# Performance work log

Measured on AMD Instinct MI355X. Metric: run time of the kernel, lower is better.

## Reference

```python
import jax, jax.numpy as jnp
import numpy as np

N, D = 8192, 256

def _gram_rbf(x, y, sigma):
    x2 = jnp.sum(x * x, axis=-1)                      # [N]
    y2 = jnp.sum(y * y, axis=-1)                      # [M]
    xy = jnp.einsum('nd,md->nm', x, y)                # [N,M] GEMM
    sq = x2[:, None] + y2[None, :] - 2.0 * xy
    return jnp.exp(-sq / sigma)

def setup_inputs() -> dict:
    key = jax.random.key(0)
    k1, k2 = jax.random.split(key)
    return {
        'input': jax.random.normal(k1, (N, D), dtype=jnp.float32),
        'target': jax.random.normal(k2, (N, D), dtype=jnp.float32) + 0.5,
        'sigma': 256,
    }

def reference(input, target, sigma):
    XX = _gram_rbf(input, input, sigma)
    YY = _gram_rbf(target, target, sigma)
    XY = _gram_rbf(input, target, sigma)
    return jnp.mean(XX) + jnp.mean(YY) - 2.0 * jnp.mean(XY)
```

## Files before the change

kernel.cpp:

```cpp
#include <hip/hip_runtime.h>
#include <hip/hip_bf16.h>
#include <stdint.h>
#include <stddef.h>


#define N_PTS   8192
#define DIM     256
#define TWO_N   16384

#define AS1 __attribute__((address_space(1)))
#define AS3 __attribute__((address_space(3)))

typedef __attribute__((ext_vector_type(4))) float f32x4;
typedef __attribute__((ext_vector_type(4))) int   i32x4;
typedef __attribute__((ext_vector_type(8))) int   i32x8;

__global__ __launch_bounds__(256) void mmd_prep(const float* __restrict__ X,
                                                const float* __restrict__ Y,
                                                const int* __restrict__ sigmap,
                                                unsigned char* __restrict__ Zf8,
                                                float* __restrict__ n2,
                                                float* __restrict__ part) {
    if (blockIdx.x == 0 && threadIdx.x < 64) part[threadIdx.x] = 0.0f;

    const int wave = threadIdx.x >> 6;
    const int lane = threadIdx.x & 63;
    const int row  = blockIdx.x * 4 + wave;

    const float* src = (row < N_PTS) ? (X + (size_t)row * DIM)
                                     : (Y + (size_t)(row - N_PTS) * DIM);
    float4 v = ((const float4*)src)[lane];

    float s = v.x * v.x + v.y * v.y + v.z * v.z + v.w * v.w;
#pragma unroll
    for (int off = 32; off; off >>= 1) s += __shfl_down(s, off, 64);
    if (lane == 0) {
        const float c2 = -1.4426950408889634f / (float)(*sigmap);
        n2[row] = c2 * s;
    }

    const int p01 = __builtin_amdgcn_cvt_pk_fp8_f32(v.x, v.y, 0, false);
    const int p23 = __builtin_amdgcn_cvt_pk_fp8_f32(v.z, v.w, 0, false);
    const unsigned int pk = ((unsigned)p01 & 0xffffu) | ((unsigned)p23 << 16);
    *(unsigned int*)(Zf8 + (size_t)row * DIM + (size_t)lane * 4) = pk;
}

__global__ __launch_bounds__(256, 4) void mmd_main(const unsigned char* __restrict__ Zf8,
                                                   const float* __restrict__ n2,
                                                   const int* __restrict__ sigmap,
                                                   float* __restrict__ part) {
    __shared__ char smem_b[32768];
    __shared__ float wsum[4];

    const int bid = (int)blockIdx.x;
    const int p   = bid >> 4;
    const int cc  = bid & 15;
    const int r0  = p;
    const int r1  = 127 - p;

    const int nT0 = (cc <= r0) ? (((r0 - cc) >> 4) + 1) : 0;
    const int nT1 = ((r1 - cc) >> 4) + 1;
    const int nS0 = nT0 * 2;
    const int nS  = nS0 + nT1 * 2;

    const int t    = threadIdx.x;
    const int wave = t >> 6;
    const int lane = t & 63;
    const int g    = lane >> 4;
    const int ml   = lane & 15;

    const float m2 = 2.8853900817779268f / (float)(*sigmap);
    const int   SC = 0x7f7f7f7f;

    const int gbase = (t >> 4) * 256 + (((t & 15) ^ (t >> 4)) * 16);
    const int lbase = t * 16;

    int rb0[2], rb1[2];
#pragma unroll
    for (int kc = 0; kc < 2; ++kc) {
        rb0[kc] = ml * 256 + (((kc * 8 + g * 2)     ^ ml) * 16);
        rb1[kc] = ml * 256 + (((kc * 8 + g * 2 + 1) ^ ml) * 16);
    }

    i32x8 af[2][2];
    float a_i[2][4];
    auto loadA = [&](int rowTile) {
        const int rowBase = rowTile * 128;
#pragma unroll
        for (int mt = 0; mt < 2; ++mt) {
            const unsigned char* rp =
                Zf8 + (size_t)(rowBase + wave * 32 + mt * 16 + ml) * 256 + g * 32;
#pragma unroll
            for (int kc = 0; kc < 2; ++kc) {
                union { i32x4 h[2]; i32x8 v; } u;
                u.h[0] = *(const i32x4*)(rp + kc * 128);
                u.h[1] = *(const i32x4*)(rp + kc * 128 + 16);
                af[mt][kc] = u.v;
            }
        }
#pragma unroll
        for (int mt = 0; mt < 2; ++mt)
#pragma unroll
            for (int rr = 0; rr < 4; ++rr)
                a_i[mt][rr] = n2[rowBase + wave * 32 + mt * 16 + g * 4 + rr];
    };

    const int firstRow = nT0 ? r0 : r1;
    loadA(firstRow);
    int curRow = firstRow;

    const f32x4 zacc = {0.0f, 0.0f, 0.0f, 0.0f};

    auto sliceCol = [&](int s, int& rowT, int& bc, int& h) {
        int si;
        if (s < nS0) { rowT = r0; si = s; }
        else         { rowT = r1; si = s - nS0; }
        bc = cc + (si >> 2) * 16 * 2;
        bc = cc + ((si >> 1) * 16);
        h  = si & 1;
    };

    {
        int rT, bc, h; sliceCol(0, rT, bc, h);
        const unsigned char* sb = Zf8 + (size_t)(bc * 128 + h * 64) * 256 + gbase;
#pragma unroll
        for (int i = 0; i < 4; ++i)
            __builtin_amdgcn_global_load_lds((const AS1 void*)(sb + i * 4096),
                                             (AS3 void*)(smem_b + i * 4096 + lbase), 16, 0, 0);
    }

    float block_acc = 0.0f;
    int cur = 0;

    for (int s = 0; s < nS; ++s) {
        int rowT, bc, h;
        sliceCol(s, rowT, bc, h);
        if (rowT != curRow) { loadA(rowT); curRow = rowT; }
        const int colBase = bc * 128 + h * 64;

        float eb[4];
#pragma unroll
        for (int nt = 0; nt < 4; ++nt)
            eb[nt] = __builtin_amdgcn_exp2f(n2[colBase + nt * 16 + ml]);

        __syncthreads();

        if (s + 1 < nS) {
            int rTN, bcN, hN;
            sliceCol(s + 1, rTN, bcN, hN);
            const unsigned char* sb =
                Zf8 + (size_t)(bcN * 128 + hN * 64) * 256 + gbase;
            char* dst = smem_b + (cur ^ 1) * 16384;
#pragma unroll
            for (int i = 0; i < 4; ++i)
                __builtin_amdgcn_global_load_lds((const AS1 void*)(sb + i * 4096),
                                                 (AS3 void*)(dst + i * 4096 + lbase), 16, 0, 0);
        }

        const char* buf = smem_b + cur * 16384;
        f32x4 acc[2][4];
#pragma unroll
        for (int nt = 0; nt < 4; ++nt) {
#pragma unroll
            for (int kc = 0; kc < 2; ++kc) {
                union { i32x4 hh[2]; i32x8 v; } u;
                u.hh[0] = *(const i32x4*)(buf + nt * 4096 + rb0[kc]);
                u.hh[1] = *(const i32x4*)(buf + nt * 4096 + rb1[kc]);
                const i32x8 bf = u.v;
#pragma unroll
                for (int mt = 0; mt < 2; ++mt)
                    acc[mt][nt] = __builtin_amdgcn_mfma_scale_f32_16x16x128_f8f6f4(
                        af[mt][kc], bf, (kc == 0) ? zacc : acc[mt][nt],
                        0, 0, 0, SC, 0, SC);
            }
        }

        float ts0 = 0.0f, ts1 = 0.0f, ts2 = 0.0f, ts3 = 0.0f;
#pragma unroll
        for (int mt = 0; mt < 2; ++mt)
#pragma unroll
            for (int nt = 0; nt < 4; ++nt) {
                const float e = eb[nt];
                ts0 = fmaf(__builtin_amdgcn_exp2f(fmaf(acc[mt][nt][0], m2, a_i[mt][0])), e, ts0);
                ts1 = fmaf(__builtin_amdgcn_exp2f(fmaf(acc[mt][nt][1], m2, a_i[mt][1])), e, ts1);
                ts2 = fmaf(__builtin_amdgcn_exp2f(fmaf(acc[mt][nt][2], m2, a_i[mt][2])), e, ts2);
                ts3 = fmaf(__builtin_amdgcn_exp2f(fmaf(acc[mt][nt][3], m2, a_i[mt][3])), e, ts3);
            }
        const float tsum = (ts0 + ts1) + (ts2 + ts3);

        const float sgn = ((bc < 64) == (rowT < 64)) ? 1.0f : -1.0f;
        const float w   = (bc == rowT) ? sgn : 2.0f * sgn;
        block_acc = fmaf(w, tsum, block_acc);
        cur ^= 1;
    }

    float s = block_acc;
#pragma unroll
    for (int off = 32; off; off >>= 1) s += __shfl_down(s, off, 64);
    if (lane == 0) wsum[wave] = s;
    __syncthreads();
    if (t == 0)
        atomicAdd(part + (bid & 63), wsum[0] + wsum[1] + wsum[2] + wsum[3]);
}

__global__ __launch_bounds__(64) void mmd_finish(const float* __restrict__ part,
                                                 float* __restrict__ out) {
    const int lane = threadIdx.x & 63;
    float s = part[lane];
#pragma unroll
    for (int off = 32; off; off >>= 1) s += __shfl_down(s, off, 64);
    if (lane == 0) out[0] = s * (1.0f / 67108864.0f);
}

extern "C" void kernel_launch(void* const* d_in, const int* in_sizes, int n_in,
                              void* d_out, int out_size, void* d_ws, size_t ws_size,
                              hipStream_t stream) {
    const float* X      = (const float*)d_in[0];
    const float* Y      = (const float*)d_in[1];
    const int*   sigmap = (const int*)d_in[2];
    float*       out    = (float*)d_out;

    unsigned char* Zf8  = (unsigned char*)d_ws;
    float*         n2   = (float*)((char*)d_ws + (size_t)TWO_N * DIM);
    float*         part = n2 + TWO_N;

    mmd_prep<<<TWO_N / 4, 256, 0, stream>>>(X, Y, sigmap, Zf8, n2, part);
    mmd_main<<<64 * 16, 256, 0, stream>>>(Zf8, n2, sigmap, part);
    mmd_finish<<<1, 64, 0, stream>>>(part, out);
}
```

Baseline: 114.1 us.

## Stagger LDS tile order per wave, pack epilogue math, simplify slice indexing

Each wave now walks the four B sub-tiles in a rotated order so that different waves hit different LDS regions at the same time. The per-slice column and row decode is replaced by an incrementally advanced byte offset. The exp epilogue uses two-wide float vectors so the compiler can emit packed FMA instructions. The final reduction drops the shared-memory barrier and has every wave do its own atomicAdd, which quadruples the atomics in exchange for removing one sync.

```diff
diff --git a/kernel.cpp b/kernel.cpp
--- a/kernel.cpp
+++ b/kernel.cpp
@@ -11,6 +11,7 @@
 #define AS1 __attribute__((address_space(1)))
 #define AS3 __attribute__((address_space(3)))
 
+typedef __attribute__((ext_vector_type(2))) float f32x2;
 typedef __attribute__((ext_vector_type(4))) float f32x4;
 typedef __attribute__((ext_vector_type(4))) int   i32x4;
 typedef __attribute__((ext_vector_type(8))) int   i32x8;
@@ -50,7 +51,6 @@
                                                    const int* __restrict__ sigmap,
                                                    float* __restrict__ part) {
     __shared__ char smem_b[32768];
-    __shared__ float wsum[4];
 
     const int bid = (int)blockIdx.x;
     const int p   = bid >> 4;
@@ -70,10 +70,19 @@
     const int ml   = lane & 15;
 
     const float m2 = 2.8853900817779268f / (float)(*sigmap);
+    const f32x2 m2v = {m2, m2};
     const int   SC = 0x7f7f7f7f;
 
     const int gbase = (t >> 4) * 256 + (((t & 15) ^ (t >> 4)) * 16);
     const int lbase = t * 16;
+
+    int ntB[4], ntE[4];
+#pragma unroll
+    for (int nt = 0; nt < 4; ++nt) {
+        const int n2v = (nt + wave) & 3;
+        ntB[nt] = n2v * 4096;
+        ntE[nt] = n2v * 16 + ml;
+    }
 
     int rb0[2], rb1[2];
 #pragma unroll
@@ -83,7 +92,7 @@
     }
 
     i32x8 af[2][2];
-    float a_i[2][4];
+    f32x2 ai01[2], ai23[2];
     auto loadA = [&](int rowTile) {
         const int rowBase = rowTile * 128;
 #pragma unroll
@@ -99,63 +108,51 @@
             }
         }
 #pragma unroll
-        for (int mt = 0; mt < 2; ++mt)
-#pragma unroll
-            for (int rr = 0; rr < 4; ++rr)
-                a_i[mt][rr] = n2[rowBase + wave * 32 + mt * 16 + g * 4 + rr];
+        for (int mt = 0; mt < 2; ++mt) {
+            const float* ap = n2 + rowBase + wave * 32 + mt * 16 + g * 4;
+            ai01[mt][0] = ap[0]; ai01[mt][1] = ap[1];
+            ai23[mt][0] = ap[2]; ai23[mt][1] = ap[3];
+        }
     };
 
     const int firstRow = nT0 ? r0 : r1;
     loadA(firstRow);
-    int curRow = firstRow;
 
     const f32x4 zacc = {0.0f, 0.0f, 0.0f, 0.0f};
-
-    auto sliceCol = [&](int s, int& rowT, int& bc, int& h) {
-        int si;
-        if (s < nS0) { rowT = r0; si = s; }
-        else         { rowT = r1; si = s - nS0; }
-        bc = cc + (si >> 2) * 16 * 2;
-        bc = cc + ((si >> 1) * 16);
-        h  = si & 1;
-    };
-
-    {
-        int rT, bc, h; sliceCol(0, rT, bc, h);
-        const unsigned char* sb = Zf8 + (size_t)(bc * 128 + h * 64) * 256 + gbase;
+    const int ccB = cc << 15;
+
+    auto stageTo = [&](char* dstBuf, int srcByte) {
+        const unsigned char* sb = Zf8 + (size_t)srcByte + gbase;
 #pragma unroll
         for (int i = 0; i < 4; ++i)
             __builtin_amdgcn_global_load_lds((const AS1 void*)(sb + i * 4096),
-                                             (AS3 void*)(smem_b + i * 4096 + lbase), 16, 0, 0);
-    }
+                                             (AS3 void*)(dstBuf + i * 4096 + lbase), 16, 0, 0);
+    };
+
+    int colByte = ccB;
+    stageTo(smem_b, colByte);
 
     float block_acc = 0.0f;
     int cur = 0;
 
     for (int s = 0; s < nS; ++s) {
-        int rowT, bc, h;
-        sliceCol(s, rowT, bc, h);
-        if (rowT != curRow) { loadA(rowT); curRow = rowT; }
-        const int colBase = bc * 128 + h * 64;
+        if (nT0 && s == nS0) loadA(r1);
+        const int rowT = (s < nS0) ? r0 : r1;
+        const int bc     = colByte >> 15;
+        const int colIdx = colByte >> 8;
 
         float eb[4];
 #pragma unroll
         for (int nt = 0; nt < 4; ++nt)
-            eb[nt] = __builtin_amdgcn_exp2f(n2[colBase + nt * 16 + ml]);
+            eb[nt] = __builtin_amdgcn_exp2f(n2[colIdx + ntE[nt]]);
+
+        const int sN = s + 1;
+        int stageByte = colByte + ((s & 1) ? 507904 : 16384);
+        if (sN == nS0) stageByte = ccB;
 
         __syncthreads();
 
-        if (s + 1 < nS) {
-            int rTN, bcN, hN;
-            sliceCol(s + 1, rTN, bcN, hN);
-            const unsigned char* sb =
-                Zf8 + (size_t)(bcN * 128 + hN * 64) * 256 + gbase;
-            char* dst = smem_b + (cur ^ 1) * 16384;
-#pragma unroll
-            for (int i = 0; i < 4; ++i)
-                __builtin_amdgcn_global_load_lds((const AS1 void*)(sb + i * 4096),
-                                                 (AS3 void*)(dst + i * 4096 + lbase), 16, 0, 0);
-        }
+        if (sN < nS) stageTo(smem_b + (cur ^ 1) * 16384, stageByte);
 
         const char* buf = smem_b + cur * 16384;
         f32x4 acc[2][4];
@@ -164,8 +161,8 @@
 #pragma unroll
             for (int kc = 0; kc < 2; ++kc) {
                 union { i32x4 hh[2]; i32x8 v; } u;
-                u.hh[0] = *(const i32x4*)(buf + nt * 4096 + rb0[kc]);
-                u.hh[1] = *(const i32x4*)(buf + nt * 4096 + rb1[kc]);
+                u.hh[0] = *(const i32x4*)(buf + ntB[nt] + rb0[kc]);
+                u.hh[1] = *(const i32x4*)(buf + ntB[nt] + rb1[kc]);
                 const i32x8 bf = u.v;
 #pragma unroll
                 for (int mt = 0; mt < 2; ++mt)
@@ -175,32 +172,38 @@
             }
         }
 
-        float ts0 = 0.0f, ts1 = 0.0f, ts2 = 0.0f, ts3 = 0.0f;
+        f32x2 ts01 = {0.0f, 0.0f}, ts23 = {0.0f, 0.0f};
 #pragma unroll
         for (int mt = 0; mt < 2; ++mt)
 #pragma unroll
             for (int nt = 0; nt < 4; ++nt) {
-                const float e = eb[nt];
-                ts0 = fmaf(__builtin_amdgcn_exp2f(fmaf(acc[mt][nt][0], m2, a_i[mt][0])), e, ts0);
-                ts1 = fmaf(__builtin_amdgcn_exp2f(fmaf(acc[mt][nt][1], m2, a_i[mt][1])), e, ts1);
-                ts2 = fmaf(__builtin_amdgcn_exp2f(fmaf(acc[mt][nt][2], m2, a_i[mt][2])), e, ts2);
-                ts3 = fmaf(__builtin_amdgcn_exp2f(fmaf(acc[mt][nt][3], m2, a_i[mt][3])), e, ts3);
+                const f32x2 lo = {acc[mt][nt][0], acc[mt][nt][1]};
+                const f32x2 hi = {acc[mt][nt][2], acc[mt][nt][3]};
+                const f32x2 tlo = __builtin_elementwise_fma(lo, m2v, ai01[mt]);
+                const f32x2 thi = __builtin_elementwise_fma(hi, m2v, ai23[mt]);
+                const f32x2 ev  = {eb[nt], eb[nt]};
+                const f32x2 elo = {__builtin_amdgcn_exp2f(tlo[0]),
+                                   __builtin_amdgcn_exp2f(tlo[1])};
+                const f32x2 ehi = {__builtin_amdgcn_exp2f(thi[0]),
+                                   __builtin_amdgcn_exp2f(thi[1])};
+                ts01 = __builtin_elementwise_fma(elo, ev, ts01);
+                ts23 = __builtin_elementwise_fma(ehi, ev, ts23);
             }
-        const float tsum = (ts0 + ts1) + (ts2 + ts3);
+        const float tsum = (ts01[0] + ts01[1]) + (ts23[0] + ts23[1]);
 
         const float sgn = ((bc < 64) == (rowT < 64)) ? 1.0f : -1.0f;
         const float w   = (bc == rowT) ? sgn : 2.0f * sgn;
         block_acc = fmaf(w, tsum, block_acc);
+
+        colByte = stageByte;
         cur ^= 1;
     }
 
     float s = block_acc;
 #pragma unroll
     for (int off = 32; off; off >>= 1) s += __shfl_down(s, off, 64);
-    if (lane == 0) wsum[wave] = s;
-    __syncthreads();
-    if (t == 0)
-        atomicAdd(part + (bid & 63), wsum[0] + wsum[1] + wsum[2] + wsum[3]);
+    if (lane == 0)
+        atomicAdd(part + (bid & 63), s);
 }
 
 __global__ __launch_bounds__(64) void mmd_finish(const float* __restrict__ part,
```

Result: slower. 119.3 us (+4.6%).
